# Performance work log

Hardware: AMD Instinct MI355X
Metric: run time of the kernel (lower is better)

## Reference

```python
import jax, jax.numpy as jnp
import numpy as np

B, S, D = 131072, 30, 4
Q = 16  # q_size for both branches
V1, V2 = 21, 11


def setup_inputs() -> dict:
    key = jax.random.key(0)
    ks = jax.random.split(key, 13)
    s = 0.5  # small init scale (~1/sqrt(in))
    inp = {
        "x": jax.random.normal(ks[0], (B, S, D), dtype=jnp.float32),
        # branch 1 (v_size=21)
        "q1_w": jax.random.normal(ks[1], (D, Q), dtype=jnp.float32) * s,
        "q1_b": jax.random.normal(ks[2], (Q,), dtype=jnp.float32) * s,
        "k1_w": jax.random.normal(ks[3], (D, Q), dtype=jnp.float32) * s,
        "k1_b": jax.random.normal(ks[4], (Q,), dtype=jnp.float32) * s,
        "v1_w": jax.random.normal(ks[5], (D, V1), dtype=jnp.float32) * s,
        "v1_b": jax.random.normal(ks[6], (V1,), dtype=jnp.float32) * s,
        # branch 2 (v_size=11)
        "q2_w": jax.random.normal(ks[7], (D, Q), dtype=jnp.float32) * s,
        "q2_b": jax.random.normal(ks[8], (Q,), dtype=jnp.float32) * s,
        "k2_w": jax.random.normal(ks[9], (D, Q), dtype=jnp.float32) * s,
        "k2_b": jax.random.normal(ks[10], (Q,), dtype=jnp.float32) * s,
        "v2_w": jax.random.normal(ks[11], (D, V2), dtype=jnp.float32) * s,
        "v2_b": jax.random.normal(ks[12], (V2,), dtype=jnp.float32) * s,
    }
    return inp


def _attn(x, qw, qb, kw, kb, vw, vb):
    # x: [B, S, D]; unscaled softmax attention + tanh (faithful to source)
    q = jnp.einsum("bsd,dq->bsq", x, qw) + qb  # [B,S,Q]
    k = jnp.einsum("bsd,dq->bsq", x, kw) + kb  # [B,S,Q]
    v = jnp.einsum("bsd,dv->bsv", x, vw) + vb  # [B,S,V]
    scores = jnp.einsum("bsq,btq->bst", q, k)  # [B,S,S], no 1/sqrt(d) scaling
    attn = jax.nn.softmax(scores, axis=-1)
    out = jnp.einsum("bst,btv->bsv", attn, v)
    return jnp.tanh(out)


def reference(x, q1_w, q1_b, k1_w, k1_b, v1_w, v1_b,
              q2_w, q2_b, k2_w, k2_b, v2_w, v2_b):
    num = _attn(x, q1_w, q1_b, k1_w, k1_b, v1_w, v1_b)  # [B,S,21]
    t = _attn(x, q2_w, q2_b, k2_w, k2_b, v2_w, v2_b)    # [B,S,11]
    return (num, t)
```

## Files before the change

### kernel.cpp

```cpp
#include <hip/hip_runtime.h>

#define SS 30
#define QQ 16
#define NV1 21
#define NV2 11
#define NVT 32
#define NB 16
#define ROWS (NB * SS)
#define CT (NB * (SS / 2))
#define THREADS 256

#define LOG2E 1.44269504088896340736f

typedef float v2f __attribute__((ext_vector_type(2)));
typedef float v4f __attribute__((ext_vector_type(4)));

__device__ __forceinline__ v2f bcast(float x) { v2f r; r.x = x; r.y = x; return r; }
__device__ __forceinline__ v2f pkfma(v2f a, v2f b, v2f c) {
    return __builtin_elementwise_fma(a, b, c);
}

__global__ __launch_bounds__(THREADS, 3) void fused_dual_attn(
    const float* __restrict__ x,
    const float* __restrict__ q1w, const float* __restrict__ q1b,
    const float* __restrict__ k1w, const float* __restrict__ k1b,
    const float* __restrict__ v1w, const float* __restrict__ v1b,
    const float* __restrict__ q2w, const float* __restrict__ q2b,
    const float* __restrict__ k2w, const float* __restrict__ k2b,
    const float* __restrict__ v2w, const float* __restrict__ v2b,
    float* __restrict__ out1, float* __restrict__ out2)
{
    __shared__ v4f xsv[ROWS];
    __shared__ float cm[2][20];
    __shared__ v4f  vwt[NVT];
    __shared__ float vbl[NVT];
    __shared__ alignas(16) float stage[ROWS * NV1];

    const int tid = threadIdx.x;
    const long long blk = blockIdx.x;

    if (tid < 40) {
        const int br = tid / 20, idx = tid % 20;
        const float* qw = br ? q2w : q1w;
        const float* qb = br ? q2b : q1b;
        const float* kw = br ? k2w : k1w;
        float acc = 0.f;
        if (idx < 16) {
            const int d = idx >> 2, e = idx & 3;
            #pragma unroll
            for (int q = 0; q < QQ; ++q) acc += qw[d * QQ + q] * kw[e * QQ + q];
        } else {
            const int e = idx - 16;
            #pragma unroll
            for (int q = 0; q < QQ; ++q) acc += kw[e * QQ + q] * qb[q];
        }
        cm[br][idx] = acc * LOG2E;
    }
    if (tid >= 64 && tid < 64 + NVT) {
        const int o = tid - 64;
        const float s2l = 2.0f * LOG2E;
        v4f w;
        if (o < NV1) {
            w.x = v1w[o] * s2l; w.y = v1w[NV1 + o] * s2l;
            w.z = v1w[2 * NV1 + o] * s2l; w.w = v1w[3 * NV1 + o] * s2l;
            vbl[o] = v1b[o] * s2l;
        } else {
            const int p = o - NV1;
            w.x = v2w[p] * s2l; w.y = v2w[NV2 + p] * s2l;
            w.z = v2w[2 * NV2 + p] * s2l; w.w = v2w[3 * NV2 + p] * s2l;
            vbl[o] = v2b[p] * s2l;
        }
        vwt[o] = w;
    }

    {
        const v4f* xg = reinterpret_cast<const v4f*>(x) + blk * ROWS;
        for (int i = tid; i < ROWS; i += THREADS)
            xsv[i] = __builtin_nontemporal_load(xg + i);
    }
    __syncthreads();

    int lrowA = 0, lrowB = 0;
    v2f h1p[4], h2p[4];
    if (tid < CT) {
        const int batch = (unsigned)tid / 15;
        const int sA = tid - batch * 15;
        lrowA = batch * SS + sA;
        lrowB = lrowA + 15;
        const v4f* xb = xsv + batch * SS;
        const v4f xA = xsv[lrowA];
        const v4f xB = xsv[lrowB];

        v2f g1p[4], g2p[4];
        #pragma unroll
        for (int e = 0; e < 4; ++e) {
            g1p[e].x = cm[0][16 + e] + xA.x * cm[0][e] + xA.y * cm[0][4 + e]
                     + xA.z * cm[0][8 + e] + xA.w * cm[0][12 + e];
            g1p[e].y = cm[0][16 + e] + xB.x * cm[0][e] + xB.y * cm[0][4 + e]
                     + xB.z * cm[0][8 + e] + xB.w * cm[0][12 + e];
            g2p[e].x = cm[1][16 + e] + xA.x * cm[1][e] + xA.y * cm[1][4 + e]
                     + xA.z * cm[1][8 + e] + xA.w * cm[1][12 + e];
            g2p[e].y = cm[1][16 + e] + xB.x * cm[1][e] + xB.y * cm[1][4 + e]
                     + xB.z * cm[1][8 + e] + xB.w * cm[1][12 + e];
        }

        v2f sum1 = {0.f, 0.f}, sum2 = {0.f, 0.f};
        #pragma unroll
        for (int e = 0; e < 4; ++e) { h1p[e] = sum1; h2p[e] = sum1; }

        #pragma unroll
        for (int t = 0; t < SS; ++t) {
            const v4f xt = xb[t];
            const v2f bx = bcast(xt.x), by = bcast(xt.y), bz = bcast(xt.z), bw = bcast(xt.w);
            v2f s1 = g1p[3] * bw;
            s1 = pkfma(g1p[2], bz, s1);
            s1 = pkfma(g1p[1], by, s1);
            s1 = pkfma(g1p[0], bx, s1);
            v2f s2 = g2p[3] * bw;
            s2 = pkfma(g2p[2], bz, s2);
            s2 = pkfma(g2p[1], by, s2);
            s2 = pkfma(g2p[0], bx, s2);
            v2f p1, p2;
            p1.x = __builtin_amdgcn_exp2f(s1.x);
            p1.y = __builtin_amdgcn_exp2f(s1.y);
            p2.x = __builtin_amdgcn_exp2f(s2.x);
            p2.y = __builtin_amdgcn_exp2f(s2.y);
            sum1 = sum1 + p1;
            sum2 = sum2 + p2;
            h1p[0] = pkfma(p1, bx, h1p[0]);
            h1p[1] = pkfma(p1, by, h1p[1]);
            h1p[2] = pkfma(p1, bz, h1p[2]);
            h1p[3] = pkfma(p1, bw, h1p[3]);
            h2p[0] = pkfma(p2, bx, h2p[0]);
            h2p[1] = pkfma(p2, by, h2p[1]);
            h2p[2] = pkfma(p2, bz, h2p[2]);
            h2p[3] = pkfma(p2, bw, h2p[3]);
        }
        v2f inv1, inv2;
        inv1.x = __builtin_amdgcn_rcpf(sum1.x);
        inv1.y = __builtin_amdgcn_rcpf(sum1.y);
        inv2.x = __builtin_amdgcn_rcpf(sum2.x);
        inv2.y = __builtin_amdgcn_rcpf(sum2.y);
        #pragma unroll
        for (int e = 0; e < 4; ++e) { h1p[e] = h1p[e] * inv1; h2p[e] = h2p[e] * inv2; }
    }

    if (tid < CT) {
        float* sA = stage + lrowA * NV1;
        float* sB = stage + lrowB * NV1;
        #pragma unroll
        for (int o = 0; o < NV1; ++o) {
            const v4f w = vwt[o];
            v2f sp = bcast(vbl[o]);
            sp = pkfma(h1p[3], bcast(w.w), sp);
            sp = pkfma(h1p[2], bcast(w.z), sp);
            sp = pkfma(h1p[1], bcast(w.y), sp);
            sp = pkfma(h1p[0], bcast(w.x), sp);
            v2f ex;
            ex.x = __builtin_amdgcn_exp2f(sp.x);
            ex.y = __builtin_amdgcn_exp2f(sp.y);
            sA[o] = fmaf(-2.0f, __builtin_amdgcn_rcpf(ex.x + 1.0f), 1.0f);
            sB[o] = fmaf(-2.0f, __builtin_amdgcn_rcpf(ex.y + 1.0f), 1.0f);
        }
    }
    __syncthreads();
    {
        const int n1 = ROWS * NV1 / 4;
        v4f* dst1 = reinterpret_cast<v4f*>(out1) + blk * n1;
        const v4f* src = reinterpret_cast<const v4f*>(stage);
        for (int i = tid; i < n1; i += THREADS)
            __builtin_nontemporal_store(src[i], dst1 + i);
    }
    __syncthreads();

    if (tid < CT) {
        float* sA = stage + lrowA * NV2;
        float* sB = stage + lrowB * NV2;
        #pragma unroll
        for (int o = 0; o < NV2; ++o) {
            const v4f w = vwt[NV1 + o];
            v2f sp = bcast(vbl[NV1 + o]);
            sp = pkfma(h2p[3], bcast(w.w), sp);
            sp = pkfma(h2p[2], bcast(w.z), sp);
            sp = pkfma(h2p[1], bcast(w.y), sp);
            sp = pkfma(h2p[0], bcast(w.x), sp);
            v2f ex;
            ex.x = __builtin_amdgcn_exp2f(sp.x);
            ex.y = __builtin_amdgcn_exp2f(sp.y);
            sA[o] = fmaf(-2.0f, __builtin_amdgcn_rcpf(ex.x + 1.0f), 1.0f);
            sB[o] = fmaf(-2.0f, __builtin_amdgcn_rcpf(ex.y + 1.0f), 1.0f);
        }
    }
    __syncthreads();
    {
        const int n2 = ROWS * NV2 / 4;
        v4f* dst2 = reinterpret_cast<v4f*>(out2) + blk * n2;
        const v4f* src = reinterpret_cast<const v4f*>(stage);
        for (int i = tid; i < n2; i += THREADS)
            __builtin_nontemporal_store(src[i], dst2 + i);
    }
}

extern "C" void kernel_launch(void* const* d_in, const int* in_sizes, int n_in,
                              void* d_out, int out_size, void* d_ws, size_t ws_size,
                              hipStream_t stream) {
    const float* x   = (const float*)d_in[0];
    const float* q1w = (const float*)d_in[1];
    const float* q1b = (const float*)d_in[2];
    const float* k1w = (const float*)d_in[3];
    const float* k1b = (const float*)d_in[4];
    const float* v1w = (const float*)d_in[5];
    const float* v1b = (const float*)d_in[6];
    const float* q2w = (const float*)d_in[7];
    const float* q2b = (const float*)d_in[8];
    const float* k2w = (const float*)d_in[9];
    const float* k2b = (const float*)d_in[10];
    const float* v2w = (const float*)d_in[11];
    const float* v2b = (const float*)d_in[12];

    const long long B = 131072LL;
    float* out1 = (float*)d_out;
    float* out2 = out1 + B * SS * NV1;

    const int nblocks = (int)(B / NB);
    fused_dual_attn<<<nblocks, THREADS, 0, stream>>>(
        x, q1w, q1b, k1w, k1b, v1w, v1b,
        q2w, q2b, k2w, k2b, v2w, v2b, out1, out2);
}
```

Before: 152.3 us.

## Split weight precompute into separate kernel and shrink blocks to one wavefront

Moves the per-block folding of Q/K and V weights into a one-block precompute kernel that writes the constants to workspace; the main kernel then only loads them. The main kernel now uses 64-thread blocks covering 4 batches each instead of 256 threads covering 16, so far more blocks are launched and barriers span a single wavefront. The intent is to drop redundant per-block weight math and get finer-grained scheduling, at the cost of a second launch, a dependency on workspace, and fewer active lanes per block (60 of 64) with more block launch overhead.

```diff
diff --git a/kernel.cpp b/kernel.cpp
--- a/kernel.cpp
+++ b/kernel.cpp
@@ -5,10 +5,9 @@
 #define NV1 21
 #define NV2 11
 #define NVT 32
-#define NB 16
-#define ROWS (NB * SS)
-#define CT (NB * (SS / 2))
-#define THREADS 256
+#define NBPB 4
+#define ROWS (NBPB * SS)
+#define THREADS 64
 
 #define LOG2E 1.44269504088896340736f
 
@@ -20,25 +19,16 @@
     return __builtin_elementwise_fma(a, b, c);
 }
 
-__global__ __launch_bounds__(THREADS, 3) void fused_dual_attn(
-    const float* __restrict__ x,
+__global__ __launch_bounds__(64) void precompute_consts(
     const float* __restrict__ q1w, const float* __restrict__ q1b,
-    const float* __restrict__ k1w, const float* __restrict__ k1b,
+    const float* __restrict__ k1w,
+    const float* __restrict__ q2w, const float* __restrict__ q2b,
+    const float* __restrict__ k2w,
     const float* __restrict__ v1w, const float* __restrict__ v1b,
-    const float* __restrict__ q2w, const float* __restrict__ q2b,
-    const float* __restrict__ k2w, const float* __restrict__ k2b,
     const float* __restrict__ v2w, const float* __restrict__ v2b,
-    float* __restrict__ out1, float* __restrict__ out2)
+    float* __restrict__ ws)
 {
-    __shared__ v4f xsv[ROWS];
-    __shared__ float cm[2][20];
-    __shared__ v4f  vwt[NVT];
-    __shared__ float vbl[NVT];
-    __shared__ alignas(16) float stage[ROWS * NV1];
-
     const int tid = threadIdx.x;
-    const long long blk = blockIdx.x;
-
     if (tid < 40) {
         const int br = tid / 20, idx = tid % 20;
         const float* qw = br ? q2w : q1w;
@@ -54,35 +44,54 @@
             #pragma unroll
             for (int q = 0; q < QQ; ++q) acc += kw[e * QQ + q] * qb[q];
         }
-        cm[br][idx] = acc * LOG2E;
-    }
-    if (tid >= 64 && tid < 64 + NVT) {
-        const int o = tid - 64;
+        ws[tid] = acc * LOG2E;
+    }
+    if (tid < NVT) {
         const float s2l = 2.0f * LOG2E;
-        v4f w;
-        if (o < NV1) {
-            w.x = v1w[o] * s2l; w.y = v1w[NV1 + o] * s2l;
-            w.z = v1w[2 * NV1 + o] * s2l; w.w = v1w[3 * NV1 + o] * s2l;
-            vbl[o] = v1b[o] * s2l;
+        v4f w; float b;
+        if (tid < NV1) {
+            w.x = v1w[tid] * s2l;          w.y = v1w[NV1 + tid] * s2l;
+            w.z = v1w[2 * NV1 + tid] * s2l; w.w = v1w[3 * NV1 + tid] * s2l;
+            b = v1b[tid] * s2l;
         } else {
-            const int p = o - NV1;
-            w.x = v2w[p] * s2l; w.y = v2w[NV2 + p] * s2l;
-            w.z = v2w[2 * NV2 + p] * s2l; w.w = v2w[3 * NV2 + p] * s2l;
-            vbl[o] = v2b[p] * s2l;
-        }
-        vwt[o] = w;
-    }
-
+            const int p = tid - NV1;
+            w.x = v2w[p] * s2l;            w.y = v2w[NV2 + p] * s2l;
+            w.z = v2w[2 * NV2 + p] * s2l;  w.w = v2w[3 * NV2 + p] * s2l;
+            b = v2b[p] * s2l;
+        }
+        reinterpret_cast<v4f*>(ws + 40)[tid] = w;
+        ws[168 + tid] = b;
+    }
+}
+
+__global__ __launch_bounds__(THREADS, 4) void fused_dual_attn(
+    const float* __restrict__ x, const float* __restrict__ ws,
+    float* __restrict__ out1, float* __restrict__ out2)
+{
+    __shared__ float cm[40];
+    __shared__ v4f  vwt[NVT];
+    __shared__ float vbl[NVT];
+    __shared__ v4f  xsv[ROWS];
+    __shared__ alignas(16) float stage[ROWS * NV1];
+
+    const int tid = threadIdx.x;
+    const long long blk = blockIdx.x;
+
+    if (tid < 40) cm[tid] = ws[tid];
+    if (tid < NVT) {
+        vwt[tid] = reinterpret_cast<const v4f*>(ws + 40)[tid];
+        vbl[tid] = ws[168 + tid];
+    }
     {
         const v4f* xg = reinterpret_cast<const v4f*>(x) + blk * ROWS;
-        for (int i = tid; i < ROWS; i += THREADS)
-            xsv[i] = __builtin_nontemporal_load(xg + i);
+        xsv[tid] = __builtin_nontemporal_load(xg + tid);
+        if (tid < ROWS - 64) xsv[64 + tid] = __builtin_nontemporal_load(xg + 64 + tid);
     }
     __syncthreads();
 
     int lrowA = 0, lrowB = 0;
     v2f h1p[4], h2p[4];
-    if (tid < CT) {
+    if (tid < 60) {
         const int batch = (unsigned)tid / 15;
         const int sA = tid - batch * 15;
         lrowA = batch * SS + sA;
@@ -94,14 +103,14 @@
         v2f g1p[4], g2p[4];
         #pragma unroll
         for (int e = 0; e < 4; ++e) {
-            g1p[e].x = cm[0][16 + e] + xA.x * cm[0][e] + xA.y * cm[0][4 + e]
-                     + xA.z * cm[0][8 + e] + xA.w * cm[0][12 + e];
-            g1p[e].y = cm[0][16 + e] + xB.x * cm[0][e] + xB.y * cm[0][4 + e]
-                     + xB.z * cm[0][8 + e] + xB.w * cm[0][12 + e];
-            g2p[e].x = cm[1][16 + e] + xA.x * cm[1][e] + xA.y * cm[1][4 + e]
-                     + xA.z * cm[1][8 + e] + xA.w * cm[1][12 + e];
-            g2p[e].y = cm[1][16 + e] + xB.x * cm[1][e] + xB.y * cm[1][4 + e]
-                     + xB.z * cm[1][8 + e] + xB.w * cm[1][12 + e];
+            g1p[e].x = cm[16 + e] + xA.x * cm[e] + xA.y * cm[4 + e]
+                     + xA.z * cm[8 + e] + xA.w * cm[12 + e];
+            g1p[e].y = cm[16 + e] + xB.x * cm[e] + xB.y * cm[4 + e]
+                     + xB.z * cm[8 + e] + xB.w * cm[12 + e];
+            g2p[e].x = cm[36 + e] + xA.x * cm[20 + e] + xA.y * cm[24 + e]
+                     + xA.z * cm[28 + e] + xA.w * cm[32 + e];
+            g2p[e].y = cm[36 + e] + xB.x * cm[20 + e] + xB.y * cm[24 + e]
+                     + xB.z * cm[28 + e] + xB.w * cm[32 + e];
         }
 
         v2f sum1 = {0.f, 0.f}, sum2 = {0.f, 0.f};
@@ -145,7 +154,7 @@
         for (int e = 0; e < 4; ++e) { h1p[e] = h1p[e] * inv1; h2p[e] = h2p[e] * inv2; }
     }
 
-    if (tid < CT) {
+    if (tid < 60) {
         float* sA = stage + lrowA * NV1;
         float* sB = stage + lrowB * NV1;
         #pragma unroll
@@ -173,7 +182,7 @@
     }
     __syncthreads();
 
-    if (tid < CT) {
+    if (tid < 60) {
         float* sA = stage + lrowA * NV2;
         float* sB = stage + lrowB * NV2;
         #pragma unroll
@@ -208,22 +217,22 @@
     const float* q1w = (const float*)d_in[1];
     const float* q1b = (const float*)d_in[2];
     const float* k1w = (const float*)d_in[3];
-    const float* k1b = (const float*)d_in[4];
     const float* v1w = (const float*)d_in[5];
     const float* v1b = (const float*)d_in[6];
     const float* q2w = (const float*)d_in[7];
     const float* q2b = (const float*)d_in[8];
     const float* k2w = (const float*)d_in[9];
-    const float* k2b = (const float*)d_in[10];
     const float* v2w = (const float*)d_in[11];
     const float* v2b = (const float*)d_in[12];
 
     const long long B = 131072LL;
     float* out1 = (float*)d_out;
     float* out2 = out1 + B * SS * NV1;
-
-    const int nblocks = (int)(B / NB);
-    fused_dual_attn<<<nblocks, THREADS, 0, stream>>>(
-        x, q1w, q1b, k1w, k1b, v1w, v1b,
-        q2w, q2b, k2w, k2b, v2w, v2b, out1, out2);
-}
+    float* ws   = (float*)d_ws;
+
+    precompute_consts<<<1, 64, 0, stream>>>(q1w, q1b, k1w, q2w, q2b, k2w,
+                                            v1w, v1b, v2w, v2b, ws);
+
+    const int nblocks = (int)(B / NBPB);
+    fused_dual_attn<<<nblocks, THREADS, 0, stream>>>(x, ws, out1, out2);
+}
```

Measured after the change: 145.5 us. -4.5%, faster.
